# Optimization experiments

Hardware: AMD Instinct MI355X
Metric: run time of the kernel (lower is better)

Reference implementation:

```python
import jax, jax.numpy as jnp
import numpy as np

# FlowNetC correlation config: kernel_size=1, so no kernel-window averaging;
# pad_size == max_displacement -> output spatial size == input spatial size.
B, C, H, W = 8, 256, 48, 64
MAX_DISP = 20   # max_displacement
STRIDE2 = 2     # displacement stride
PAD = 20        # pad_size
GRID_RAD = MAX_DISP // STRIDE2            # 10
GRID_W = 2 * GRID_RAD + 1                 # 21 -> 441 displacement channels


def setup_inputs() -> dict:
    key = jax.random.key(0)
    k1, k2 = jax.random.split(key)
    return {
        "input1": jax.random.normal(k1, (B, C, H, W), dtype=jnp.float32),
        "input2": jax.random.normal(k2, (B, C, H, W), dtype=jnp.float32),
    }


def _correlation(input1, input2):
    b, c, h, w = input1.shape
    p2 = jnp.pad(input2, ((0, 0), (0, 0), (PAD, PAD), (PAD, PAD)))
    # Displacement start offsets into the padded map. dy-major ordering matches
    # the CUDA kernel: top_channel = dy_idx * GRID_W + dx_idx.
    d = np.arange(-GRID_RAD, GRID_RAD + 1) * STRIDE2 + PAD  # [21]
    offs = np.stack(np.meshgrid(d, d, indexing="ij"), axis=-1).reshape(-1, 2)
    offs = jnp.asarray(offs, dtype=jnp.int32)  # [441, 2] (dy, dx)
    sumelems = jnp.float32(c)  # kernel_size^2 * C with kernel_size=1

    def step(carry, o):
        shifted = jax.lax.dynamic_slice(p2, (0, 0, o[0], o[1]), (b, c, h, w))
        # mean over channels of elementwise product -> [B, H, W]
        return carry, jnp.sum(input1 * shifted, axis=1) / sumelems

    _, ys = jax.lax.scan(step, 0, offs)          # [441, B, H, W]
    return jnp.transpose(ys, (1, 0, 2, 3))       # [B, 441, H, W]


def reference(input1, input2):
    return _correlation(input1, input2)
```

## Files before the change

### kernel.cpp

```cpp
#include <hip/hip_runtime.h>

typedef __bf16 bf16x8 __attribute__((ext_vector_type(8)));
typedef float f32x4 __attribute__((ext_vector_type(4)));
typedef float f32x16 __attribute__((ext_vector_type(16)));

#define CC 256
#define HH 48
#define WW 64
#define HW (HH * WW)
#define NB 8
#define GW 21

__global__ __launch_bounds__(256) void prep_kernel(const float* __restrict__ in1,
                                                   const float* __restrict__ in2,
                                                   unsigned short* __restrict__ o1,
                                                   unsigned short* __restrict__ o2)
{
    __shared__ float lds[CC * 33];
    int blk  = blockIdx.x;
    int sel  = (blk >= 768);
    int blk2 = sel ? blk - 768 : blk;
    int b  = blk2 & 7;
    int st = blk2 >> 3;
    int s0 = st * 32;
    const float* src = sel ? in2 : in1;
    unsigned short* dst = sel ? o2 : o1;
    float scale = sel ? 1.0f : (1.0f / 256.0f);

    int t = threadIdx.x;
    int sidx  = t & 31;
    int cbase = t >> 5;
    const float* sb = src + (size_t)b * CC * HW + s0;
    #pragma unroll
    for (int p = 0; p < 32; ++p) {
        int c = cbase + p * 8;
        lds[c * 33 + sidx] = sb[(size_t)c * HW + sidx] * scale;
    }
    __syncthreads();

    int y  = s0 >> 6;
    int xb = s0 & 63;
    int s  = t & 31;
    int c8 = t >> 5;
    unsigned short* db = dst + (size_t)(b * HH + y) * 32 * 64 * 8;
    int x = xb + s;
    int xoff = (x & 1) * 32 + (x >> 1);
    #pragma unroll
    for (int it = 0; it < 4; ++it) {
        int cblk = it * 8 + c8;
        unsigned dw[4];
        #pragma unroll
        for (int d = 0; d < 4; ++d) {
            unsigned u0 = __builtin_bit_cast(unsigned, lds[(cblk * 8 + 2 * d) * 33 + s]);
            u0 += 0x7fffu + ((u0 >> 16) & 1u);
            unsigned u1 = __builtin_bit_cast(unsigned, lds[(cblk * 8 + 2 * d + 1) * 33 + s]);
            u1 += 0x7fffu + ((u1 >> 16) & 1u);
            dw[d] = (u0 >> 16) | (u1 & 0xffff0000u);
        }
        *(uint4*)(db + ((size_t)cblk * 64 + xoff) * 8) =
            make_uint4(dw[0], dw[1], dw[2], dw[3]);
    }
}

__global__ __launch_bounds__(256, 2) void corr_kernel(const unsigned short* __restrict__ in1F,
                                                      const unsigned short* __restrict__ in2F,
                                                      float* __restrict__ out)
{
    __shared__ unsigned char smem[65536];
    unsigned short* Bl = (unsigned short*)smem;

    int blk = blockIdx.x;
    int b   = blk & 7;
    int r   = blk >> 3;
    int yi  = r / 3;
    int jg  = r - yi * 3;
    int ys0 = yi - 20;
    int ys1 = ys0 + 2;

    int tid  = threadIdx.x;
    int w    = tid >> 6;
    int lane = tid & 63;
    int q    = jg * 4 + w;
    int yo   = ys0 + 20 - 4 * q;
    int j0   = 2 * q;
    bool v1  = (q <= 9);
    bool wvalid = (q <= 10) && (yo >= 0) && (yo < HH);
    bool vs0 = (ys0 >= 0) && (ys0 < HH);
    bool vs1 = (ys1 >= 0) && (ys1 < HH);

    float* orow0 = out + (((size_t)(b * 441 + j0 * GW)) * HH + yo) * WW;
    float* orow1 = orow0 + (size_t)GW * HW;

    if (!vs0 && !vs1) {
        if (wvalid) {
            #pragma unroll
            for (int jx = 0; jx < GW; ++jx)
                __builtin_nontemporal_store(0.0f, orow0 + (size_t)jx * HW + lane);
            if (v1) {
                #pragma unroll
                for (int jx = 0; jx < GW; ++jx)
                    __builtin_nontemporal_store(0.0f, orow1 + (size_t)jx * HW + lane);
            }
        }
        return;
    }

    int l31 = lane & 31;
    int q2  = lane >> 5;

    const unsigned short* arow = in1F
        + ((size_t)(b * HH + (wvalid ? yo : 0)) * 32 + q2) * 512 + (size_t)l31 * 8;

    bf16x8 Ab[4][2], Bb[2][2][2];
    if (wvalid) {
        #pragma unroll
        for (int kr = 0; kr < 3; ++kr)
            #pragma unroll
            for (int p = 0; p < 2; ++p)
                Ab[kr][p] = *(const bf16x8*)(arow + (size_t)kr * 1024 + p * 256);
    }

    {
        uint4* dst = (uint4*)Bl;
        if (vs0) {
            const uint4* s = (const uint4*)(in2F + (size_t)(b * HH + ys0) * 16384);
            #pragma unroll
            for (int i = 0; i < 8; ++i) dst[i * 256 + tid] = s[i * 256 + tid];
        }
        if (vs1) {
            const uint4* s = (const uint4*)(in2F + (size_t)(b * HH + ys1) * 16384);
            #pragma unroll
            for (int i = 0; i < 8; ++i) dst[2048 + i * 256 + tid] = s[i * 256 + tid];
        }
    }
    __syncthreads();

    f32x16 acc[2][2];
    if (wvalid) {
        const unsigned short* brow = Bl + q2 * 512 + (size_t)l31 * 8;

        #pragma unroll
        for (int jj = 0; jj < 2; ++jj)
            #pragma unroll
            for (int p = 0; p < 2; ++p)
                acc[jj][p] = (f32x16)(0.0f);

        #pragma unroll
        for (int jj = 0; jj < 2; ++jj)
            #pragma unroll
            for (int p = 0; p < 2; ++p)
                Bb[0][jj][p] = *(const bf16x8*)(brow + jj * 16384 + p * 256);

        #pragma unroll
        for (int kk = 0; kk < 16; ++kk) {
            if (kk < 13) {
                #pragma unroll
                for (int p = 0; p < 2; ++p)
                    Ab[(kk + 3) & 3][p] =
                        *(const bf16x8*)(arow + (size_t)(kk + 3) * 1024 + p * 256);
            }
            if (kk < 15) {
                #pragma unroll
                for (int jj = 0; jj < 2; ++jj)
                    #pragma unroll
                    for (int p = 0; p < 2; ++p)
                        Bb[(kk + 1) & 1][jj][p] =
                            *(const bf16x8*)(brow + jj * 16384 + (size_t)(kk + 1) * 1024 + p * 256);
            }
            #pragma unroll
            for (int jj = 0; jj < 2; ++jj)
                #pragma unroll
                for (int p = 0; p < 2; ++p)
                    acc[jj][p] = __builtin_amdgcn_mfma_f32_32x32x16_bf16(
                        Ab[kk & 3][p], Bb[kk & 1][jj][p], acc[jj][p], 0, 0, 0);
        }
    }

    __syncthreads();
    if (!wvalid) return;

    float* dtw = (float*)smem + w * 2304;
    int xe = lane >> 1;
    int pe = lane & 1;
    #pragma unroll
    for (int jj = 0; jj < 2; ++jj) {
        if (jj == 1 && !v1) continue;
        bool vsj = jj ? vs1 : vs0;
        float* orow = jj ? orow1 : orow0;
        #pragma unroll
        for (int p = 0; p < 2; ++p)
            #pragma unroll
            for (int rq = 0; rq < 4; ++rq) {
                f32x4 v = { acc[jj][p][4 * rq], acc[jj][p][4 * rq + 1],
                            acc[jj][p][4 * rq + 2], acc[jj][p][4 * rq + 3] };
                *(f32x4*)(dtw + (size_t)(p * 32 + l31) * 36 + rq * 8 + q2 * 4) = v;
            }
        #pragma unroll
        for (int jx = 0; jx < GW; ++jx) {
            int ce = xe + jx - 10;
            float val = (vsj && ce >= 0 && ce < 32)
                      ? dtw[(size_t)(pe * 32 + ce) * 36 + xe] : 0.0f;
            __builtin_nontemporal_store(val, orow + (size_t)jx * HW + lane);
        }
    }
}

extern "C" void kernel_launch(void* const* d_in, const int* in_sizes, int n_in,
                              void* d_out, int out_size, void* d_ws, size_t ws_size,
                              hipStream_t stream)
{
    (void)in_sizes; (void)n_in; (void)out_size; (void)ws_size;
    const float* in1 = (const float*)d_in[0];
    const float* in2 = (const float*)d_in[1];
    float* out = (float*)d_out;

    unsigned short* in1F = (unsigned short*)d_ws;
    unsigned short* in2F = in1F + (size_t)NB * HW * CC;

    prep_kernel<<<dim3(1536), dim3(256), 0, stream>>>(in1, in2, in1F, in2F);
    corr_kernel<<<dim3(NB * 88 * 3), dim3(256), 0, stream>>>(in1F, in2F, out);
}
```

Before: 117.5 us.

## Merge three blocks per input-row pair into one 6-wave block with direct LDS loads

Each block now covers all 11 q-groups for a given pair of input2 rows, using 6 waves with up to two q-groups each, instead of three blocks of 4 waves each. The input2 rows are loaded into LDS once per block rather than three times, and they arrive through global_load_lds direct-to-LDS transfers. The epilogue staging area gets its own LDS region, which removes the second barrier. The cost is more registers per wave for the doubled accumulators, 118 KB of LDS per block that probably limits a CU to one block, and an uneven load because some waves hold only one q-group.

```diff
diff --git a/kernel.cpp b/kernel.cpp
--- a/kernel.cpp
+++ b/kernel.cpp
@@ -10,6 +10,11 @@
 #define HW (HH * WW)
 #define NB 8
 #define GW 21
+
+#define GLOAD_LDS16(g, l)                                                     \
+    __builtin_amdgcn_global_load_lds(                                         \
+        (const __attribute__((address_space(1))) unsigned int*)(g),           \
+        (__attribute__((address_space(3))) unsigned int*)(l), 16, 0, 0)
 
 __global__ __launch_bounds__(256) void prep_kernel(const float* __restrict__ in1,
                                                    const float* __restrict__ in2,
@@ -62,145 +67,158 @@
     }
 }
 
-__global__ __launch_bounds__(256, 2) void corr_kernel(const unsigned short* __restrict__ in1F,
+__global__ __launch_bounds__(384, 2) void corr_kernel(const unsigned short* __restrict__ in1F,
                                                       const unsigned short* __restrict__ in2F,
                                                       float* __restrict__ out)
 {
-    __shared__ unsigned char smem[65536];
+    __shared__ unsigned char smem[120832];
     unsigned short* Bl = (unsigned short*)smem;
 
     int blk = blockIdx.x;
     int b   = blk & 7;
-    int r   = blk >> 3;
-    int yi  = r / 3;
-    int jg  = r - yi * 3;
+    int yi  = blk >> 3;
     int ys0 = yi - 20;
     int ys1 = ys0 + 2;
+    bool vs0 = (ys0 >= 0) && (ys0 < HH);
+    bool vs1 = (ys1 >= 0) && (ys1 < HH);
 
     int tid  = threadIdx.x;
     int w    = tid >> 6;
     int lane = tid & 63;
-    int q    = jg * 4 + w;
-    int yo   = ys0 + 20 - 4 * q;
-    int j0   = 2 * q;
-    bool v1  = (q <= 9);
-    bool wvalid = (q <= 10) && (yo >= 0) && (yo < HH);
-    bool vs0 = (ys0 >= 0) && (ys0 < HH);
-    bool vs1 = (ys1 >= 0) && (ys1 < HH);
-
-    float* orow0 = out + (((size_t)(b * 441 + j0 * GW)) * HH + yo) * WW;
-    float* orow1 = orow0 + (size_t)GW * HW;
+    int l31  = lane & 31;
+    int q2   = lane >> 5;
+
+    int q_[2];  q_[0] = w;  q_[1] = w + 6;
+    int yo_[2]; yo_[0] = ys0 + 20 - 4 * q_[0];  yo_[1] = ys0 + 20 - 4 * q_[1];
+    bool qv_[2];
+    qv_[0] = (yo_[0] >= 0) && (yo_[0] < HH);
+    qv_[1] = (q_[1] <= 10) && (yo_[1] >= 0) && (yo_[1] < HH);
 
     if (!vs0 && !vs1) {
-        if (wvalid) {
-            #pragma unroll
-            for (int jx = 0; jx < GW; ++jx)
-                __builtin_nontemporal_store(0.0f, orow0 + (size_t)jx * HW + lane);
-            if (v1) {
+        #pragma unroll
+        for (int qi = 0; qi < 2; ++qi) {
+            if (!qv_[qi]) continue;
+            #pragma unroll
+            for (int jj = 0; jj < 2; ++jj) {
+                int j = 2 * q_[qi] + jj;
+                if (j > 20) continue;
+                float* orow = out + (((size_t)(b * 441 + j * GW)) * HH + yo_[qi]) * WW;
                 #pragma unroll
                 for (int jx = 0; jx < GW; ++jx)
-                    __builtin_nontemporal_store(0.0f, orow1 + (size_t)jx * HW + lane);
+                    __builtin_nontemporal_store(0.0f, orow + (size_t)jx * HW + lane);
             }
         }
         return;
     }
 
-    int l31 = lane & 31;
-    int q2  = lane >> 5;
-
-    const unsigned short* arow = in1F
-        + ((size_t)(b * HH + (wvalid ? yo : 0)) * 32 + q2) * 512 + (size_t)l31 * 8;
-
-    bf16x8 Ab[4][2], Bb[2][2][2];
-    if (wvalid) {
-        #pragma unroll
-        for (int kr = 0; kr < 3; ++kr)
+    const unsigned short* ar_[2];
+    ar_[0] = in1F + (size_t)(b * HH + (qv_[0] ? yo_[0] : 0)) * 16384 + q2 * 512 + l31 * 8;
+    ar_[1] = in1F + (size_t)(b * HH + (qv_[1] ? yo_[1] : 0)) * 16384 + q2 * 512 + l31 * 8;
+
+    bf16x8 Ab[4][2][2], Bb[2][2][2];
+    #pragma unroll
+    for (int s = 0; s < 3; ++s)
+        #pragma unroll
+        for (int qi = 0; qi < 2; ++qi)
+            if (qv_[qi])
+                #pragma unroll
+                for (int p = 0; p < 2; ++p)
+                    Ab[s][qi][p] = *(const bf16x8*)(ar_[qi] + s * 1024 + p * 256);
+
+    for (int i = w; i < 64; i += 6) {
+        int row = i >> 5, ch = i & 31;
+        bool v = row ? vs1 : vs0;
+        if (v) {
+            const unsigned short* src = in2F
+                + (size_t)(b * HH + (row ? ys1 : ys0)) * 16384 + ch * 512 + lane * 8;
+            GLOAD_LDS16(src, Bl + row * 16384 + ch * 512);
+        }
+    }
+    __syncthreads();
+
+    f32x16 acc[2][2][2];
+    #pragma unroll
+    for (int qi = 0; qi < 2; ++qi)
+        #pragma unroll
+        for (int jj = 0; jj < 2; ++jj)
             #pragma unroll
             for (int p = 0; p < 2; ++p)
-                Ab[kr][p] = *(const bf16x8*)(arow + (size_t)kr * 1024 + p * 256);
-    }
-
-    {
-        uint4* dst = (uint4*)Bl;
-        if (vs0) {
-            const uint4* s = (const uint4*)(in2F + (size_t)(b * HH + ys0) * 16384);
-            #pragma unroll
-            for (int i = 0; i < 8; ++i) dst[i * 256 + tid] = s[i * 256 + tid];
-        }
-        if (vs1) {
-            const uint4* s = (const uint4*)(in2F + (size_t)(b * HH + ys1) * 16384);
-            #pragma unroll
-            for (int i = 0; i < 8; ++i) dst[2048 + i * 256 + tid] = s[i * 256 + tid];
-        }
-    }
-    __syncthreads();
-
-    f32x16 acc[2][2];
-    if (wvalid) {
-        const unsigned short* brow = Bl + q2 * 512 + (size_t)l31 * 8;
-
-        #pragma unroll
-        for (int jj = 0; jj < 2; ++jj)
+                acc[qi][jj][p] = (f32x16)(0.0f);
+
+    int lofs = q2 * 512 + l31 * 8;
+    #pragma unroll
+    for (int jj = 0; jj < 2; ++jj)
+        if (jj ? vs1 : vs0)
             #pragma unroll
             for (int p = 0; p < 2; ++p)
-                acc[jj][p] = (f32x16)(0.0f);
-
-        #pragma unroll
-        for (int jj = 0; jj < 2; ++jj)
-            #pragma unroll
-            for (int p = 0; p < 2; ++p)
-                Bb[0][jj][p] = *(const bf16x8*)(brow + jj * 16384 + p * 256);
-
-        #pragma unroll
-        for (int kk = 0; kk < 16; ++kk) {
-            if (kk < 13) {
-                #pragma unroll
-                for (int p = 0; p < 2; ++p)
-                    Ab[(kk + 3) & 3][p] =
-                        *(const bf16x8*)(arow + (size_t)(kk + 3) * 1024 + p * 256);
-            }
-            if (kk < 15) {
-                #pragma unroll
-                for (int jj = 0; jj < 2; ++jj)
+                Bb[0][jj][p] = *(const bf16x8*)(Bl + jj * 16384 + lofs + p * 256);
+
+    #pragma unroll
+    for (int kk = 0; kk < 16; ++kk) {
+        if (kk < 13) {
+            #pragma unroll
+            for (int qi = 0; qi < 2; ++qi)
+                if (qv_[qi])
+                    #pragma unroll
+                    for (int p = 0; p < 2; ++p)
+                        Ab[(kk + 3) & 3][qi][p] =
+                            *(const bf16x8*)(ar_[qi] + (size_t)(kk + 3) * 1024 + p * 256);
+        }
+        if (kk < 15) {
+            #pragma unroll
+            for (int jj = 0; jj < 2; ++jj)
+                if (jj ? vs1 : vs0)
                     #pragma unroll
                     for (int p = 0; p < 2; ++p)
                         Bb[(kk + 1) & 1][jj][p] =
-                            *(const bf16x8*)(brow + jj * 16384 + (size_t)(kk + 1) * 1024 + p * 256);
-            }
-            #pragma unroll
-            for (int jj = 0; jj < 2; ++jj)
-                #pragma unroll
-                for (int p = 0; p < 2; ++p)
-                    acc[jj][p] = __builtin_amdgcn_mfma_f32_32x32x16_bf16(
-                        Ab[kk & 3][p], Bb[kk & 1][jj][p], acc[jj][p], 0, 0, 0);
-        }
-    }
-
-    __syncthreads();
-    if (!wvalid) return;
-
-    float* dtw = (float*)smem + w * 2304;
+                            *(const bf16x8*)(Bl + jj * 16384 + (kk + 1) * 1024 + lofs + p * 256);
+        }
+        #pragma unroll
+        for (int qi = 0; qi < 2; ++qi)
+            #pragma unroll
+            for (int jj = 0; jj < 2; ++jj) {
+                bool live = qv_[qi] && (jj ? vs1 : vs0);
+                if (live)
+                    #pragma unroll
+                    for (int p = 0; p < 2; ++p)
+                        acc[qi][jj][p] = __builtin_amdgcn_mfma_f32_32x32x16_bf16(
+                            Ab[kk & 3][qi][p], Bb[kk & 1][jj][p], acc[qi][jj][p], 0, 0, 0);
+            }
+    }
+
+    float* dtw = (float*)(smem + 65536) + w * 2304;
     int xe = lane >> 1;
     int pe = lane & 1;
     #pragma unroll
-    for (int jj = 0; jj < 2; ++jj) {
-        if (jj == 1 && !v1) continue;
-        bool vsj = jj ? vs1 : vs0;
-        float* orow = jj ? orow1 : orow0;
-        #pragma unroll
-        for (int p = 0; p < 2; ++p)
-            #pragma unroll
-            for (int rq = 0; rq < 4; ++rq) {
-                f32x4 v = { acc[jj][p][4 * rq], acc[jj][p][4 * rq + 1],
-                            acc[jj][p][4 * rq + 2], acc[jj][p][4 * rq + 3] };
-                *(f32x4*)(dtw + (size_t)(p * 32 + l31) * 36 + rq * 8 + q2 * 4) = v;
-            }
-        #pragma unroll
-        for (int jx = 0; jx < GW; ++jx) {
-            int ce = xe + jx - 10;
-            float val = (vsj && ce >= 0 && ce < 32)
-                      ? dtw[(size_t)(pe * 32 + ce) * 36 + xe] : 0.0f;
-            __builtin_nontemporal_store(val, orow + (size_t)jx * HW + lane);
+    for (int qi = 0; qi < 2; ++qi) {
+        if (!qv_[qi]) continue;
+        #pragma unroll
+        for (int jj = 0; jj < 2; ++jj) {
+            int j = 2 * q_[qi] + jj;
+            if (j > 20) continue;
+            float* orow = out + (((size_t)(b * 441 + j * GW)) * HH + yo_[qi]) * WW;
+            bool vsj = jj ? vs1 : vs0;
+            if (!vsj) {
+                #pragma unroll
+                for (int jx = 0; jx < GW; ++jx)
+                    __builtin_nontemporal_store(0.0f, orow + (size_t)jx * HW + lane);
+                continue;
+            }
+            #pragma unroll
+            for (int p = 0; p < 2; ++p)
+                #pragma unroll
+                for (int rq = 0; rq < 4; ++rq) {
+                    f32x4 v = { acc[qi][jj][p][4 * rq], acc[qi][jj][p][4 * rq + 1],
+                                acc[qi][jj][p][4 * rq + 2], acc[qi][jj][p][4 * rq + 3] };
+                    *(f32x4*)(dtw + (size_t)(p * 32 + l31) * 36 + rq * 8 + q2 * 4) = v;
+                }
+            #pragma unroll
+            for (int jx = 0; jx < GW; ++jx) {
+                int ce = xe + jx - 10;
+                float val = (ce >= 0 && ce < 32)
+                          ? dtw[(size_t)(pe * 32 + ce) * 36 + xe] : 0.0f;
+                __builtin_nontemporal_store(val, orow + (size_t)jx * HW + lane);
+            }
         }
     }
 }
@@ -218,5 +236,5 @@
     unsigned short* in2F = in1F + (size_t)NB * HW * CC;
 
     prep_kernel<<<dim3(1536), dim3(256), 0, stream>>>(in1, in2, in1F, in2F);
-    corr_kernel<<<dim3(NB * 88 * 3), dim3(256), 0, stream>>>(in1F, in2F, out);
+    corr_kernel<<<dim3(NB * 88), dim3(384), 0, stream>>>(in1F, in2F, out);
 }
```

Result: no change. 118.6 us (+1.0%).

## Load B operands directly from global and shrink blocks to two waves

Applied to the files above, without the earlier changes.

The correlation kernel no longer stages the two input2 rows into 64 KB of shared memory behind a block barrier. Each wave now streams its B fragments straight from global or L2 in a 4-deep register ring, like the A operand. Blocks drop to 128 threads with a 6-way split over displacement rows, so LDS use falls to the 18 KB epilogue transpose buffer, which should allow more resident blocks. The trade-off is that the same in2 rows are fetched from L2 by many waves instead of once per block, and the prefetch ring adds register pressure.

```diff
diff --git a/kernel.cpp b/kernel.cpp
--- a/kernel.cpp
+++ b/kernel.cpp
@@ -62,131 +62,95 @@
     }
 }
 
-__global__ __launch_bounds__(256, 2) void corr_kernel(const unsigned short* __restrict__ in1F,
+__global__ __launch_bounds__(128, 2) void corr_kernel(const unsigned short* __restrict__ in1F,
                                                       const unsigned short* __restrict__ in2F,
                                                       float* __restrict__ out)
 {
-    __shared__ unsigned char smem[65536];
-    unsigned short* Bl = (unsigned short*)smem;
+    __shared__ float dts[2][2304];
 
     int blk = blockIdx.x;
     int b   = blk & 7;
     int r   = blk >> 3;
-    int yi  = r / 3;
-    int jg  = r - yi * 3;
+    int yi  = r / 6;
+    int qh  = r - yi * 6;
     int ys0 = yi - 20;
     int ys1 = ys0 + 2;
 
     int tid  = threadIdx.x;
     int w    = tid >> 6;
     int lane = tid & 63;
-    int q    = jg * 4 + w;
+    int q    = qh + 6 * w;
     int yo   = ys0 + 20 - 4 * q;
-    int j0   = 2 * q;
-    bool v1  = (q <= 9);
-    bool wvalid = (q <= 10) && (yo >= 0) && (yo < HH);
-    bool vs0 = (ys0 >= 0) && (ys0 < HH);
-    bool vs1 = (ys1 >= 0) && (ys1 < HH);
 
-    float* orow0 = out + (((size_t)(b * 441 + j0 * GW)) * HH + yo) * WW;
-    float* orow1 = orow0 + (size_t)GW * HW;
+    if (q > 10 || yo < 0 || yo >= HH) return;
 
-    if (!vs0 && !vs1) {
-        if (wvalid) {
-            #pragma unroll
-            for (int jx = 0; jx < GW; ++jx)
-                __builtin_nontemporal_store(0.0f, orow0 + (size_t)jx * HW + lane);
-            if (v1) {
-                #pragma unroll
-                for (int jx = 0; jx < GW; ++jx)
-                    __builtin_nontemporal_store(0.0f, orow1 + (size_t)jx * HW + lane);
-            }
-        }
-        return;
-    }
+    bool vs_[2];
+    vs_[0] = (ys0 >= 0) && (ys0 < HH);
+    vs_[1] = (ys1 >= 0) && (ys1 < HH);
+    int j0 = 2 * q;
 
     int l31 = lane & 31;
     int q2  = lane >> 5;
+    int lofs = q2 * 512 + l31 * 8;
 
-    const unsigned short* arow = in1F
-        + ((size_t)(b * HH + (wvalid ? yo : 0)) * 32 + q2) * 512 + (size_t)l31 * 8;
+    const unsigned short* ar = in1F + (size_t)(b * HH + yo) * 16384 + lofs;
+    const unsigned short* br_[2];
+    br_[0] = in2F + (size_t)(b * HH + (vs_[0] ? ys0 : 0)) * 16384 + lofs;
+    br_[1] = in2F + (size_t)(b * HH + (vs_[1] ? ys1 : 0)) * 16384 + lofs;
 
-    bf16x8 Ab[4][2], Bb[2][2][2];
-    if (wvalid) {
+    bf16x8 Ab[4][2], Bb[4][2][2];
+    #pragma unroll
+    for (int s = 0; s < 3; ++s) {
         #pragma unroll
-        for (int kr = 0; kr < 3; ++kr)
+        for (int p = 0; p < 2; ++p)
+            Ab[s][p] = *(const bf16x8*)(ar + s * 1024 + p * 256);
+        #pragma unroll
+        for (int jj = 0; jj < 2; ++jj)
+            if (vs_[jj])
+                #pragma unroll
+                for (int p = 0; p < 2; ++p)
+                    Bb[s][jj][p] = *(const bf16x8*)(br_[jj] + s * 1024 + p * 256);
+    }
+
+    f32x16 acc[2][2];
+    #pragma unroll
+    for (int jj = 0; jj < 2; ++jj)
+        #pragma unroll
+        for (int p = 0; p < 2; ++p)
+            acc[jj][p] = (f32x16)(0.0f);
+
+    #pragma unroll
+    for (int kk = 0; kk < 16; ++kk) {
+        if (kk < 13) {
             #pragma unroll
             for (int p = 0; p < 2; ++p)
-                Ab[kr][p] = *(const bf16x8*)(arow + (size_t)kr * 1024 + p * 256);
-    }
-
-    {
-        uint4* dst = (uint4*)Bl;
-        if (vs0) {
-            const uint4* s = (const uint4*)(in2F + (size_t)(b * HH + ys0) * 16384);
+                Ab[(kk + 3) & 3][p] =
+                    *(const bf16x8*)(ar + (size_t)(kk + 3) * 1024 + p * 256);
             #pragma unroll
-            for (int i = 0; i < 8; ++i) dst[i * 256 + tid] = s[i * 256 + tid];
+            for (int jj = 0; jj < 2; ++jj)
+                if (vs_[jj])
+                    #pragma unroll
+                    for (int p = 0; p < 2; ++p)
+                        Bb[(kk + 3) & 3][jj][p] =
+                            *(const bf16x8*)(br_[jj] + (size_t)(kk + 3) * 1024 + p * 256);
         }
-        if (vs1) {
-            const uint4* s = (const uint4*)(in2F + (size_t)(b * HH + ys1) * 16384);
-            #pragma unroll
-            for (int i = 0; i < 8; ++i) dst[2048 + i * 256 + tid] = s[i * 256 + tid];
-        }
-    }
-    __syncthreads();
-
-    f32x16 acc[2][2];
-    if (wvalid) {
-        const unsigned short* brow = Bl + q2 * 512 + (size_t)l31 * 8;
-
         #pragma unroll
         for (int jj = 0; jj < 2; ++jj)
-            #pragma unroll
-            for (int p = 0; p < 2; ++p)
-                acc[jj][p] = (f32x16)(0.0f);
-
-        #pragma unroll
-        for (int jj = 0; jj < 2; ++jj)
-            #pragma unroll
-            for (int p = 0; p < 2; ++p)
-                Bb[0][jj][p] = *(const bf16x8*)(brow + jj * 16384 + p * 256);
-
-        #pragma unroll
-        for (int kk = 0; kk < 16; ++kk) {
-            if (kk < 13) {
-                #pragma unroll
-                for (int p = 0; p < 2; ++p)
-                    Ab[(kk + 3) & 3][p] =
-                        *(const bf16x8*)(arow + (size_t)(kk + 3) * 1024 + p * 256);
-            }
-            if (kk < 15) {
-                #pragma unroll
-                for (int jj = 0; jj < 2; ++jj)
-                    #pragma unroll
-                    for (int p = 0; p < 2; ++p)
-                        Bb[(kk + 1) & 1][jj][p] =
-                            *(const bf16x8*)(brow + jj * 16384 + (size_t)(kk + 1) * 1024 + p * 256);
-            }
-            #pragma unroll
-            for (int jj = 0; jj < 2; ++jj)
+            if (vs_[jj])
                 #pragma unroll
                 for (int p = 0; p < 2; ++p)
                     acc[jj][p] = __builtin_amdgcn_mfma_f32_32x32x16_bf16(
-                        Ab[kk & 3][p], Bb[kk & 1][jj][p], acc[jj][p], 0, 0, 0);
-        }
+                        Ab[kk & 3][p], Bb[kk & 3][jj][p], acc[jj][p], 0, 0, 0);
     }
 
-    __syncthreads();
-    if (!wvalid) return;
-
-    float* dtw = (float*)smem + w * 2304;
+    float* dtw = dts[w];
     int xe = lane >> 1;
     int pe = lane & 1;
     #pragma unroll
     for (int jj = 0; jj < 2; ++jj) {
-        if (jj == 1 && !v1) continue;
-        bool vsj = jj ? vs1 : vs0;
-        float* orow = jj ? orow1 : orow0;
+        int j = j0 + jj;
+        if (j > 20) continue;
+        float* orow = out + (((size_t)(b * 441 + j * GW)) * HH + yo) * WW;
         #pragma unroll
         for (int p = 0; p < 2; ++p)
             #pragma unroll
@@ -198,7 +162,7 @@
         #pragma unroll
         for (int jx = 0; jx < GW; ++jx) {
             int ce = xe + jx - 10;
-            float val = (vsj && ce >= 0 && ce < 32)
+            float val = (ce >= 0 && ce < 32)
                       ? dtw[(size_t)(pe * 32 + ce) * 36 + xe] : 0.0f;
             __builtin_nontemporal_store(val, orow + (size_t)jx * HW + lane);
         }
@@ -218,5 +182,5 @@
     unsigned short* in2F = in1F + (size_t)NB * HW * CC;
 
     prep_kernel<<<dim3(1536), dim3(256), 0, stream>>>(in1, in2, in1F, in2F);
-    corr_kernel<<<dim3(NB * 88 * 3), dim3(256), 0, stream>>>(in1F, in2F, out);
+    corr_kernel<<<dim3(NB * 88 * 6), dim3(128), 0, stream>>>(in1F, in2F, out);
 }
```

Result: no change. 115.8 us (-1.4%).
